# Kernel optimization log

Measured on AMD Instinct MI355X. Metric: run time of the kernel, lower is better.

Reference implementation:

```python
import jax, jax.numpy as jnp
import numpy as np

B, N, DIN, DOUT, DOP = 64, 512, 256, 256, 64
LN_EPS = 1e-5
NEG_SLOPE = 0.2


def setup_inputs() -> dict:
    key = jax.random.key(0)
    ks = jax.random.split(key, 16)
    stdv = 1.0 / np.sqrt(DOUT)

    def lin(k, shape, fan_in):
        # torch nn.Linear default init: U(-1/sqrt(fan_in), 1/sqrt(fan_in))
        bound = 1.0 / np.sqrt(fan_in)
        return jax.random.uniform(k, shape, jnp.float32, -bound, bound)

    return {
        "inputs": jax.random.normal(ks[0], (B, N, DIN), jnp.float32),
        "adj": jax.random.uniform(ks[1], (B, N, N), jnp.float32),
        "op_emb": jax.random.normal(ks[2], (B, N, DOP), jnp.float32),
        # DenseGraphFlow params
        "dgf_W": jax.random.uniform(ks[3], (DIN, DOUT), jnp.float32, -stdv, stdv),
        "dgf_b": jax.random.uniform(ks[4], (DOUT,), jnp.float32, -stdv, stdv),
        "dgf_opW": lin(ks[5], (DOUT, DOP), DOP),
        "dgf_opb": lin(ks[6], (DOUT,), DOP),
        # GraphAttentionLayer params
        "Wk": lin(ks[7], (DOUT, DIN), DIN),
        "Wv": lin(ks[8], (DOUT, DIN), DIN),
        "Wq": lin(ks[9], (DOUT, DIN), DIN),
        "a_w": lin(ks[10], (DOUT,), DOUT),
        "gat_opW": lin(ks[11], (DOUT, DOP), DOP),
        "gat_opb": lin(ks[12], (DOUT,), DOP),
        "ln_g": jnp.ones((DOUT,), jnp.float32),
        "ln_b": jnp.zeros((DOUT,), jnp.float32),
    }


def reference(inputs, adj, op_emb, dgf_W, dgf_b, dgf_opW, dgf_opb,
              Wk, Wv, Wq, a_w, gat_opW, gat_opb, ln_g, ln_b):
    # ----- DenseGraphFlow branch -----
    support = jnp.einsum('bni,io->bno', inputs, dgf_W)            # [B,N,DOUT]
    gate_d = jax.nn.sigmoid(op_emb @ dgf_opW.T + dgf_opb)        # [B,N,DOUT]
    dense = gate_d * jnp.einsum('bij,bjo->bio', adj, support)
    dense = dense + support + dgf_b                               # residual + bias

    # ----- GraphAttentionLayer branch -----
    Whk = inputs @ Wk.T                                           # [B,N,DOUT]
    Whv = inputs @ Wv.T
    Whq = inputs @ Wq.T
    # torch einsum 'balm,beam->belm' (a=1) builds Whq[b,e,:]*Whk[b,l,:];
    # a(.) contracts the feature dim -> equivalent fused score:
    scores = jnp.einsum('bem,blm,m->bel', Whq, Whk, a_w)
    scores = scores / jnp.sqrt(jnp.float32(DOUT))                 # attention_rescale
    alpha = jax.nn.leaky_relu(scores, NEG_SLOPE) * adj            # mask by multiply
    attn = jax.nn.softmax(alpha, axis=-1)                         # softmax over l (neighbors)
    gate_g = jax.nn.sigmoid(op_emb @ gat_opW.T + gat_opb)
    h_prime = gate_g * jnp.einsum('bel,blm->bem', attn, Whv)
    # LayerNorm over last dim
    mu = jnp.mean(h_prime, axis=-1, keepdims=True)
    var = jnp.var(h_prime, axis=-1, keepdims=True)
    gat = (h_prime - mu) * jax.lax.rsqrt(var + LN_EPS) * ln_g + ln_b

    return (dense + gat) * 0.5
```

## Files before the change

### kernel.cpp

```cpp
#include <hip/hip_runtime.h>
#include <cstdint>
#include <cstddef>

typedef unsigned short u16;
typedef unsigned int   u32;
typedef __attribute__((ext_vector_type(8))) short bf16x8;
typedef __attribute__((ext_vector_type(4))) float f32x4;

#define MFMA16(a,b,c) __builtin_amdgcn_mfma_f32_16x16x32_bf16((a),(b),(c),0,0,0)

__device__ __forceinline__ float bf2f(u16 h){
  union { u32 u; float f; } v; v.u = ((u32)h) << 16; return v.f;
}
__device__ __forceinline__ u16 f2bf(float f){
  union { float f; u32 u; } v; v.f = f;
  u32 u = v.u + 0x7FFFu + ((v.u >> 16) & 1u);
  return (u16)(u >> 16);
}
__device__ __forceinline__ float ldf(const void* p, int i, u32 isf32){
  return isf32 ? ((const float*)p)[i] : bf2f(((const u16*)p)[i]);
}

__global__ void kD_detect(const u16* __restrict__ raw, u32* __restrict__ flag)
{
  const int lane = threadIdx.x & 63;
  const float v = bf2f(raw[lane]);
  const unsigned long long big = __ballot(fabsf(v) > 1.0e6f);
  if (lane == 0) flag[0] = (big != 0ull) ? 1u : 0u;
}

__global__ void kC_conv(const void* __restrict__ src, u16* __restrict__ dst,
                        int n, const u32* __restrict__ flag)
{
  const int i8 = (blockIdx.x * 256 + threadIdx.x) << 3;
  if (i8 >= n) return;
  if (flag[0]) {
    const float4 a = ((const float4*)src)[i8 >> 2];
    const float4 b = ((const float4*)src)[(i8 >> 2) + 1];
    u16 o[8] = { f2bf(a.x), f2bf(a.y), f2bf(a.z), f2bf(a.w),
                 f2bf(b.x), f2bf(b.y), f2bf(b.z), f2bf(b.w) };
    *(uint4*)&dst[i8] = *(const uint4*)o;
  } else {
    ((uint4*)dst)[i8 >> 3] = ((const uint4*)src)[i8 >> 3];
  }
}

__global__ void kP_params(const void* dgf_opW, const void* gat_opW,
                          const void* dgf_b,   const void* dgf_opb,
                          const void* gat_opb, const void* ln_g,
                          const void* ln_b,    u16* __restrict__ PB,
                          const u32* __restrict__ flag)
{
  const int i = blockIdx.x * 256 + threadIdx.x;
  if (i >= 34048) return;
  const u32 f = flag[0];
  float v;
  if      (i < 16384) v = ldf(dgf_opW, i, f);
  else if (i < 32768) v = ldf(gat_opW, i - 16384, f);
  else if (i < 33024) v = ldf(dgf_b,   i - 32768, f);
  else if (i < 33280) v = ldf(dgf_opb, i - 33024, f);
  else if (i < 33536) v = ldf(gat_opb, i - 33280, f);
  else if (i < 33792) v = ldf(ln_g,    i - 33536, f);
  else                v = ldf(ln_b,    i - 33792, f);
  PB[i] = f2bf(v);
}

__global__ void k0_wcat(const void* dgfW, const void* Wk, const void* Wv,
                        const void* Wq, const void* aw, u16* __restrict__ Wcat,
                        const u32* __restrict__ flag)
{
  const int o = blockIdx.x;
  const int i = threadIdx.x;
  const u32 f = flag[0];
  float v;
  if (o < 256)       v = ldf(dgfW, i * 256 + o, f);
  else if (o < 512)  v = ldf(Wk, (o - 256) * 256 + i, f);
  else if (o < 768)  v = ldf(Wv, (o - 512) * 256 + i, f);
  else               v = ldf(Wq, (o - 768) * 256 + i, f) * ldf(aw, o - 768, f) * 0.0625f;
  Wcat[o * 256 + i] = f2bf(v);
}

__global__ __launch_bounds__(256, 2)
void k1_proj(const u16* __restrict__ X, const u16* __restrict__ W,
             u16* __restrict__ P, u16* __restrict__ T)
{
  __shared__ __align__(16) u16 ldsA[128 * 64];
  __shared__ __align__(16) u16 ldsB[128 * 64];
  const int bt = blockIdx.x;
  const int ct = blockIdx.y;
  const int r0 = bt << 7;
  const bool swapped = (ct == 4) | (ct == 5) | (ct >= 8);
  const int wbase = (ct < 8) ? (ct << 7) : ((ct - 8) << 7);
  const int tid = threadIdx.x;
  const int wave = tid >> 6;
  const int lane = tid & 63;
  const int wm = wave >> 1, wn = wave & 1;

  f32x4 acc[4][4];
#pragma unroll
  for (int i = 0; i < 4; ++i)
#pragma unroll
    for (int j = 0; j < 4; ++j) acc[i][j] = f32x4{0.f, 0.f, 0.f, 0.f};

  for (int kt = 0; kt < 4; ++kt) {
    __syncthreads();
#pragma unroll
    for (int s = 0; s < 4; ++s) {
      const int slot = ((wave * 4 + s) << 6) + lane;
      const int m = slot >> 3, c = slot & 7;
      const int kb = c ^ (m & 7);
      *(uint4*)&ldsA[slot << 3] =
          *(const uint4*)(X + (r0 + m) * 256 + (kt << 6) + (kb << 3));
      *(uint4*)&ldsB[slot << 3] =
          *(const uint4*)(W + (wbase + m) * 256 + (kt << 6) + (kb << 3));
    }
    __syncthreads();
#pragma unroll
    for (int ks = 0; ks < 2; ++ks) {
      const int kb = (ks << 2) + (lane >> 4);
      bf16x8 fa[4], fb[4];
#pragma unroll
      for (int i = 0; i < 4; ++i) {
        const int m = (wm << 6) + (i << 4) + (lane & 15);
        fa[i] = *(const bf16x8*)&ldsA[((m << 3) + (kb ^ (m & 7))) << 3];
        const int n = (wn << 6) + (i << 4) + (lane & 15);
        fb[i] = *(const bf16x8*)&ldsB[((n << 3) + (kb ^ (n & 7))) << 3];
      }
      if (!swapped) {
#pragma unroll
        for (int i = 0; i < 4; ++i)
#pragma unroll
          for (int j = 0; j < 4; ++j)
            acc[i][j] = MFMA16(fa[i], fb[j], acc[i][j]);
      } else {
#pragma unroll
        for (int i = 0; i < 4; ++i)
#pragma unroll
          for (int j = 0; j < 4; ++j)
            acc[i][j] = MFMA16(fb[i], fa[j], acc[i][j]);
      }
    }
  }

  if (!swapped) {
    const int pcb = (ct < 4) ? (ct << 7) : ((ct - 2) << 7);
#pragma unroll
    for (int i = 0; i < 4; ++i) {
      const int row = r0 + (wm << 6) + (i << 4) + ((lane >> 4) << 2);
#pragma unroll
      for (int j = 0; j < 4; ++j) {
        const int col = pcb + (wn << 6) + (j << 4) + (lane & 15);
#pragma unroll
        for (int r = 0; r < 4; ++r)
          P[(row + r) * 768 + col] = f2bf(acc[i][j][r]);
      }
    }
  } else {
    const int trb = (wbase >= 512) ? (wbase - 256) : wbase;
    const int b = r0 >> 9;
    const int e0 = r0 & 511;
    u16* Tb = T + ((size_t)b << 18);
#pragma unroll
    for (int i = 0; i < 4; ++i) {
      const int trow = trb + (wn << 6) + (i << 4) + ((lane >> 4) << 2);
#pragma unroll
      for (int j = 0; j < 4; ++j) {
        const int e = e0 + (wm << 6) + (j << 4) + (lane & 15);
#pragma unroll
        for (int r = 0; r < 4; ++r)
          Tb[((trow + r) << 9) + e] = f2bf(acc[i][j][r]);
      }
    }
  }
}

__global__ __launch_bounds__(256, 2)
void k2_gates(const u16* __restrict__ OP, const u16* __restrict__ PB,
              u16* __restrict__ G)
{
  __shared__ __align__(16) u16 ldsA[128 * 64];
  __shared__ __align__(16) u16 ldsB[128 * 64];
  const int bt = blockIdx.x, ct = blockIdx.y;
  const int r0 = bt << 7;
  const u16* Wp = (ct < 2) ? (PB + (ct << 7) * 64) : (PB + 16384 + ((ct - 2) << 7) * 64);
  const u16* Bp = (ct < 2) ? (PB + 33024 + (ct << 7)) : (PB + 33280 + ((ct - 2) << 7));
  const int tid = threadIdx.x, wave = tid >> 6, lane = tid & 63;
  const int wm = wave >> 1, wn = wave & 1;

  f32x4 acc[4][4];
#pragma unroll
  for (int i = 0; i < 4; ++i)
#pragma unroll
    for (int j = 0; j < 4; ++j) acc[i][j] = f32x4{0.f, 0.f, 0.f, 0.f};

#pragma unroll
  for (int s = 0; s < 4; ++s) {
    const int slot = ((wave * 4 + s) << 6) + lane;
    const int m = slot >> 3, c = slot & 7;
    const int kb = c ^ (m & 7);
    *(uint4*)&ldsA[slot << 3] = *(const uint4*)(OP + (r0 + m) * 64 + (kb << 3));
    *(uint4*)&ldsB[slot << 3] = *(const uint4*)(Wp + m * 64 + (kb << 3));
  }
  __syncthreads();
#pragma unroll
  for (int ks = 0; ks < 2; ++ks) {
    const int kb = (ks << 2) + (lane >> 4);
    bf16x8 fa[4], fb[4];
#pragma unroll
    for (int i = 0; i < 4; ++i) {
      const int m = (wm << 6) + (i << 4) + (lane & 15);
      fa[i] = *(const bf16x8*)&ldsA[((m << 3) + (kb ^ (m & 7))) << 3];
      const int n = (wn << 6) + (i << 4) + (lane & 15);
      fb[i] = *(const bf16x8*)&ldsB[((n << 3) + (kb ^ (n & 7))) << 3];
    }
#pragma unroll
    for (int i = 0; i < 4; ++i)
#pragma unroll
      for (int j = 0; j < 4; ++j)
        acc[i][j] = MFMA16(fa[i], fb[j], acc[i][j]);
  }
#pragma unroll
  for (int i = 0; i < 4; ++i) {
    const int row = r0 + (wm << 6) + (i << 4) + ((lane >> 4) << 2);
#pragma unroll
    for (int j = 0; j < 4; ++j) {
      const int cw = (wn << 6) + (j << 4) + (lane & 15);
      const float bias = bf2f(Bp[cw]);
      const int col = (ct << 7) + cw;
#pragma unroll
      for (int r = 0; r < 4; ++r) {
        const float x = acc[i][j][r] + bias;
        G[((row + r) << 9) + col] = f2bf(1.0f / (1.0f + __expf(-x)));
      }
    }
  }
}

__global__ __launch_bounds__(256, 2)
void k3_scores(const u16* __restrict__ P, const u16* __restrict__ adj,
               u16* __restrict__ E)
{
  __shared__ __align__(16) u16 ldsA[128 * 64];
  __shared__ __align__(16) u16 ldsB[128 * 64];
  const int lt = blockIdx.x, et = blockIdx.y, b = blockIdx.z;
  const int e0 = et << 7, l0 = lt << 7;
  const int tid = threadIdx.x, wave = tid >> 6, lane = tid & 63;
  const int wm = wave >> 1, wn = wave & 1;
  const int rowQ = (b << 9) + e0;
  const int rowK = (b << 9) + l0;

  f32x4 acc[4][4];
#pragma unroll
  for (int i = 0; i < 4; ++i)
#pragma unroll
    for (int j = 0; j < 4; ++j) acc[i][j] = f32x4{0.f, 0.f, 0.f, 0.f};

  for (int kt = 0; kt < 4; ++kt) {
    __syncthreads();
#pragma unroll
    for (int s = 0; s < 4; ++s) {
      const int slot = ((wave * 4 + s) << 6) + lane;
      const int m = slot >> 3, c = slot & 7;
      const int kb = c ^ (m & 7);
      *(uint4*)&ldsA[slot << 3] =
          *(const uint4*)(P + (rowQ + m) * 768 + 512 + (kt << 6) + (kb << 3));
      *(uint4*)&ldsB[slot << 3] =
          *(const uint4*)(P + (rowK + m) * 768 + 256 + (kt << 6) + (kb << 3));
    }
    __syncthreads();
#pragma unroll
    for (int ks = 0; ks < 2; ++ks) {
      const int kb = (ks << 2) + (lane >> 4);
      bf16x8 fa[4], fb[4];
#pragma unroll
      for (int i = 0; i < 4; ++i) {
        const int m = (wm << 6) + (i << 4) + (lane & 15);
        fa[i] = *(const bf16x8*)&ldsA[((m << 3) + (kb ^ (m & 7))) << 3];
        const int n = (wn << 6) + (i << 4) + (lane & 15);
        fb[i] = *(const bf16x8*)&ldsB[((n << 3) + (kb ^ (n & 7))) << 3];
      }
#pragma unroll
      for (int i = 0; i < 4; ++i)
#pragma unroll
        for (int j = 0; j < 4; ++j)
          acc[i][j] = MFMA16(fa[i], fb[j], acc[i][j]);
    }
  }
#pragma unroll
  for (int i = 0; i < 4; ++i) {
    const int e = e0 + (wm << 6) + (i << 4) + ((lane >> 4) << 2);
#pragma unroll
    for (int j = 0; j < 4; ++j) {
      const int l = l0 + (wn << 6) + (j << 4) + (lane & 15);
#pragma unroll
      for (int r = 0; r < 4; ++r) {
        const int idx = (((b << 9) + e + r) << 9) + l;
        const float a = bf2f(adj[idx]);
        float s = acc[i][j][r];
        s = (s > 0.0f ? s : 0.2f * s) * a;
        E[idx] = f2bf(__expf(s));
      }
    }
  }
}

__global__ void k3b_rowsum(const u16* __restrict__ E, float* __restrict__ S)
{
  const int row = (blockIdx.x << 2) + (threadIdx.x >> 6);
  const int lane = threadIdx.x & 63;
  const uint4 v = *(const uint4*)(const void*)(E + ((size_t)row << 9) + (lane << 3));
  float s = 0.0f;
  const u32 w[4] = {v.x, v.y, v.z, v.w};
#pragma unroll
  for (int q = 0; q < 4; ++q)
    s += bf2f((u16)(w[q] & 0xFFFFu)) + bf2f((u16)(w[q] >> 16));
#pragma unroll
  for (int m = 32; m >= 1; m >>= 1) s += __shfl_xor(s, m, 64);
  if (lane == 0) S[row] = s;
}

__global__ __launch_bounds__(256, 2)
void k4_out(const u16* __restrict__ P, const u16* __restrict__ T,
            const u16* __restrict__ E, const u16* __restrict__ adj,
            const float* __restrict__ S, const u16* __restrict__ G,
            const u16* __restrict__ PB, void* __restrict__ out,
            const u32* __restrict__ flag)
{
  __shared__ __align__(16) u16 ldsA[64 * 64];
  __shared__ __align__(16) u16 ldsB[256 * 64];
  __shared__ float red[64][4];
  const int et = blockIdx.x, b = blockIdx.y;
  const int e0 = et << 6;
  const int tid = threadIdx.x, wave = tid >> 6, lane = tid & 63;
  const int wm = wave >> 1, wn = wave & 1;
  const size_t abase = ((size_t)((b << 9) + e0)) << 9;
  const u16* Ea  = E + abase;
  const u16* Aa  = adj + abase;
  const u16* Tb  = T + ((size_t)b << 18);
  const u16* WhvT = Tb + (256 << 9);
  const u16* SupT = Tb;
  const u16* dgf_b = PB + 32768;
  const u16* ln_g  = PB + 33536;
  const u16* ln_b  = PB + 33792;
  const u32 isf32 = flag[0];

  f32x4 acc[2][2][8];
#pragma unroll
  for (int p = 0; p < 2; ++p)
#pragma unroll
    for (int i = 0; i < 2; ++i)
#pragma unroll
      for (int j = 0; j < 8; ++j) acc[p][i][j] = f32x4{0.f, 0.f, 0.f, 0.f};

#pragma unroll
  for (int ph = 0; ph < 2; ++ph) {
    const u16* Ag = ph ? Aa : Ea;
    const u16* Bg = ph ? SupT : WhvT;
    for (int lt = 0; lt < 8; ++lt) {
      __syncthreads();
#pragma unroll
      for (int s2 = 0; s2 < 2; ++s2) {
        const int slot = ((wave * 2 + s2) << 6) + lane;
        const int m = slot >> 3, c = slot & 7;
        const int kb = c ^ (m & 7);
        *(uint4*)&ldsA[slot << 3] =
            *(const uint4*)(Ag + (m << 9) + (lt << 6) + (kb << 3));
      }
#pragma unroll
      for (int s2 = 0; s2 < 8; ++s2) {
        const int slot = ((wave * 8 + s2) << 6) + lane;
        const int m = slot >> 3, c = slot & 7;
        const int kb = c ^ (m & 7);
        *(uint4*)&ldsB[slot << 3] =
            *(const uint4*)(Bg + (m << 9) + (lt << 6) + (kb << 3));
      }
      __syncthreads();
#pragma unroll
      for (int ks = 0; ks < 2; ++ks) {
        const int kb = (ks << 2) + (lane >> 4);
        bf16x8 fa[2];
#pragma unroll
        for (int i = 0; i < 2; ++i) {
          const int m = (wm << 5) + (i << 4) + (lane & 15);
          fa[i] = *(const bf16x8*)&ldsA[((m << 3) + (kb ^ (m & 7))) << 3];
        }
#pragma unroll
        for (int j = 0; j < 8; ++j) {
          const int n = (wn << 7) + (j << 4) + (lane & 15);
          const bf16x8 fb = *(const bf16x8*)&ldsB[((n << 3) + (kb ^ (n & 7))) << 3];
          acc[ph][0][j] = MFMA16(fa[0], fb, acc[ph][0][j]);
          acc[ph][1][j] = MFMA16(fa[1], fb, acc[ph][1][j]);
        }
      }
    }
  }

  const int cb = wn << 7;
  float lng[8], lnb[8], dgb[8];
#pragma unroll
  for (int j = 0; j < 8; ++j) {
    const int col = cb + (j << 4) + (lane & 15);
    lng[j] = bf2f(ln_g[col]);
    lnb[j] = bf2f(ln_b[col]);
    dgb[j] = bf2f(dgf_b[col]);
  }
#pragma unroll
  for (int i = 0; i < 2; ++i) {
#pragma unroll
    for (int r = 0; r < 4; ++r) {
      const int rl = (wm << 5) + (i << 4) + ((lane >> 4) << 2) + r;
      const int grow = (b << 9) + e0 + rl;
      const float invS = 1.0f / S[grow];
      float ps = 0.0f, pq = 0.0f;
#pragma unroll
      for (int j = 0; j < 8; ++j) {
        const int col = cb + (j << 4) + (lane & 15);
        const float gg = bf2f(G[((size_t)grow << 9) + 256 + col]);
        const float hp = gg * acc[0][i][j][r] * invS;
        acc[0][i][j][r] = hp;
        ps += hp; pq += hp * hp;
      }
#pragma unroll
      for (int m = 1; m < 16; m <<= 1) {
        ps += __shfl_xor(ps, m, 64);
        pq += __shfl_xor(pq, m, 64);
      }
      if ((lane & 15) == 0) { red[rl][wn << 1] = ps; red[rl][(wn << 1) + 1] = pq; }
    }
  }
  __syncthreads();
#pragma unroll
  for (int i = 0; i < 2; ++i) {
#pragma unroll
    for (int r = 0; r < 4; ++r) {
      const int rl = (wm << 5) + (i << 4) + ((lane >> 4) << 2) + r;
      const int grow = (b << 9) + e0 + rl;
      const float mean = (red[rl][0] + red[rl][2]) * (1.0f / 256.0f);
      const float ex2  = (red[rl][1] + red[rl][3]) * (1.0f / 256.0f);
      const float rstd = rsqrtf(ex2 - mean * mean + 1e-5f);
#pragma unroll
      for (int j = 0; j < 8; ++j) {
        const int col = cb + (j << 4) + (lane & 15);
        const float gat = (acc[0][i][j][r] - mean) * rstd * lng[j] + lnb[j];
        const float gd = bf2f(G[((size_t)grow << 9) + col]);
        const float sup = bf2f(P[grow * 768 + col]);
        const float dense = gd * acc[1][i][j][r] + sup + dgb[j];
        const float o = 0.5f * (dense + gat);
        if (isf32) ((float*)out)[grow * 256 + col] = o;
        else       ((u16*)out)[grow * 256 + col] = f2bf(o);
      }
    }
  }
}

extern "C" void kernel_launch(void* const* d_in, const int* in_sizes, int n_in,
                              void* d_out, int out_size, void* d_ws, size_t ws_size,
                              hipStream_t stream)
{
  (void)in_sizes; (void)n_in; (void)out_size; (void)ws_size;
  const void* inputs  = d_in[0];
  const void* adj     = d_in[1];
  const void* op_emb  = d_in[2];
  const void* dgf_W   = d_in[3];
  const void* dgf_b   = d_in[4];
  const void* dgf_opW = d_in[5];
  const void* dgf_opb = d_in[6];
  const void* Wk      = d_in[7];
  const void* Wv      = d_in[8];
  const void* Wq      = d_in[9];
  const void* a_w     = d_in[10];
  const void* gat_opW = d_in[11];
  const void* gat_opb = d_in[12];
  const void* ln_g    = d_in[13];
  const void* ln_b    = d_in[14];
  char* ws = (char*)d_ws;

  u16*  P    = (u16*)(ws);
  u16*  T    = (u16*)(ws + 50331648ull);
  u16*  E    = (u16*)(ws + 83886080ull);
  u16*  G    = (u16*)(ws + 117440512ull);
  u16*  Cadj = (u16*)(ws + 150994944ull);
  u16*  Cin  = (u16*)(ws + 184549376ull);
  u16*  Cop  = (u16*)(ws + 201326592ull);
  u16*  Wcat = (u16*)(ws + 205520896ull);
  u16*  PB   = (u16*)(ws + 206045184ull);
  float* Srw = (float*)(ws + 206114816ull);
  u32*  flag = (u32*)(ws + 206245888ull);

  kD_detect <<<dim3(1),       dim3(64),  0, stream>>>((const u16*)inputs, flag);
  kC_conv   <<<dim3(4096),    dim3(256), 0, stream>>>(inputs, Cin,  8388608, flag);
  kC_conv   <<<dim3(1024),    dim3(256), 0, stream>>>(op_emb, Cop,  2097152, flag);
  kC_conv   <<<dim3(8192),    dim3(256), 0, stream>>>(adj,    Cadj, 16777216, flag);
  kP_params <<<dim3(134),     dim3(256), 0, stream>>>(dgf_opW, gat_opW, dgf_b,
                                                      dgf_opb, gat_opb, ln_g, ln_b,
                                                      PB, flag);
  k0_wcat   <<<dim3(1024),    dim3(256), 0, stream>>>(dgf_W, Wk, Wv, Wq, a_w,
                                                      Wcat, flag);
  k1_proj   <<<dim3(256, 10), dim3(256), 0, stream>>>(Cin, Wcat, P, T);
  k2_gates  <<<dim3(256, 4),  dim3(256), 0, stream>>>(Cop, PB, G);
  k3_scores <<<dim3(4, 4, 64),dim3(256), 0, stream>>>(P, Cadj, E);
  k3b_rowsum<<<dim3(8192),    dim3(256), 0, stream>>>(E, Srw);
  k4_out    <<<dim3(8, 64),   dim3(256), 0, stream>>>(P, T, E, Cadj, Srw, G,
                                                      PB, d_out, flag);
}
```

Before: 332.1 us.

## Fuse softmax row-sum into output GEMM and load MFMA fragments directly

Removes the separate row-sum kernel and computes the softmax denominator inside k4_out with an extra MFMA against a vector of ones. The output kernel now uses 32-row tiles (twice as many blocks), drops LDS staging and reads MFMA fragments straight from global memory, and fuses the two GEMM phases into one K loop. This saves a launch and a full re-read of E and raises occupancy. The cost is uncoalesced global fragment loads with no LDS reuse, so the B operands are fetched more often from cache.

```diff
diff --git a/kernel.cpp b/kernel.cpp
--- a/kernel.cpp
+++ b/kernel.cpp
@@ -304,120 +304,102 @@
   }
 }
 
-__global__ void k3b_rowsum(const u16* __restrict__ E, float* __restrict__ S)
-{
-  const int row = (blockIdx.x << 2) + (threadIdx.x >> 6);
-  const int lane = threadIdx.x & 63;
-  const uint4 v = *(const uint4*)(const void*)(E + ((size_t)row << 9) + (lane << 3));
-  float s = 0.0f;
-  const u32 w[4] = {v.x, v.y, v.z, v.w};
-#pragma unroll
-  for (int q = 0; q < 4; ++q)
-    s += bf2f((u16)(w[q] & 0xFFFFu)) + bf2f((u16)(w[q] >> 16));
-#pragma unroll
-  for (int m = 32; m >= 1; m >>= 1) s += __shfl_xor(s, m, 64);
-  if (lane == 0) S[row] = s;
-}
-
-__global__ __launch_bounds__(256, 2)
+__global__ __launch_bounds__(256, 3)
 void k4_out(const u16* __restrict__ P, const u16* __restrict__ T,
             const u16* __restrict__ E, const u16* __restrict__ adj,
-            const float* __restrict__ S, const u16* __restrict__ G,
-            const u16* __restrict__ PB, void* __restrict__ out,
-            const u32* __restrict__ flag)
-{
-  __shared__ __align__(16) u16 ldsA[64 * 64];
-  __shared__ __align__(16) u16 ldsB[256 * 64];
-  __shared__ float red[64][4];
+            const u16* __restrict__ G, const u16* __restrict__ PB,
+            void* __restrict__ out, const u32* __restrict__ flag)
+{
+  __shared__ float red[32][8];
   const int et = blockIdx.x, b = blockIdx.y;
-  const int e0 = et << 6;
-  const int tid = threadIdx.x, wave = tid >> 6, lane = tid & 63;
-  const int wm = wave >> 1, wn = wave & 1;
+  const int e0 = et << 5;
+  const int tid = threadIdx.x;
+  const int wn = tid >> 6;
+  const int lane = tid & 63;
+  const int lr = lane & 15;
+  const int kc = (lane >> 4) << 3;
   const size_t abase = ((size_t)((b << 9) + e0)) << 9;
-  const u16* Ea  = E + abase;
-  const u16* Aa  = adj + abase;
-  const u16* Tb  = T + ((size_t)b << 18);
-  const u16* WhvT = Tb + (256 << 9);
-  const u16* SupT = Tb;
+
+  const u16* pE[2]; const u16* pA[2]; const u16* pBv[4]; const u16* pBs[4];
+#pragma unroll
+  for (int i = 0; i < 2; ++i) {
+    const size_t ro = abase + ((size_t)((i << 4) + lr) << 9) + kc;
+    pE[i] = E + ro;
+    pA[i] = adj + ro;
+  }
+  const u16* Tb = T + ((size_t)b << 18);
+#pragma unroll
+  for (int j = 0; j < 4; ++j) {
+    const int n = (wn << 6) + (j << 4) + lr;
+    pBv[j] = Tb + ((size_t)(256 + n) << 9) + kc;
+    pBs[j] = Tb + ((size_t)n << 9) + kc;
+  }
+
+  f32x4 acc0[2][4], acc1[2][4], accS[2];
+#pragma unroll
+  for (int i = 0; i < 2; ++i) {
+    accS[i] = f32x4{0.f, 0.f, 0.f, 0.f};
+#pragma unroll
+    for (int j = 0; j < 4; ++j) {
+      acc0[i][j] = f32x4{0.f, 0.f, 0.f, 0.f};
+      acc1[i][j] = f32x4{0.f, 0.f, 0.f, 0.f};
+    }
+  }
+  const short onebf = (short)0x3F80;
+  const bf16x8 ones = {onebf, onebf, onebf, onebf, onebf, onebf, onebf, onebf};
+
+  for (int ks = 0; ks < 16; ++ks) {
+    const int off = ks << 5;
+    bf16x8 fae[2], faa[2], fbv[4], fbs[4];
+#pragma unroll
+    for (int i = 0; i < 2; ++i) {
+      fae[i] = *(const bf16x8*)(pE[i] + off);
+      faa[i] = *(const bf16x8*)(pA[i] + off);
+    }
+#pragma unroll
+    for (int j = 0; j < 4; ++j) {
+      fbv[j] = *(const bf16x8*)(pBv[j] + off);
+      fbs[j] = *(const bf16x8*)(pBs[j] + off);
+    }
+#pragma unroll
+    for (int i = 0; i < 2; ++i) {
+#pragma unroll
+      for (int j = 0; j < 4; ++j) {
+        acc0[i][j] = MFMA16(fae[i], fbv[j], acc0[i][j]);
+        acc1[i][j] = MFMA16(faa[i], fbs[j], acc1[i][j]);
+      }
+      accS[i] = MFMA16(fae[i], ones, accS[i]);
+    }
+  }
+
   const u16* dgf_b = PB + 32768;
   const u16* ln_g  = PB + 33536;
   const u16* ln_b  = PB + 33792;
   const u32 isf32 = flag[0];
 
-  f32x4 acc[2][2][8];
-#pragma unroll
-  for (int p = 0; p < 2; ++p)
-#pragma unroll
-    for (int i = 0; i < 2; ++i)
-#pragma unroll
-      for (int j = 0; j < 8; ++j) acc[p][i][j] = f32x4{0.f, 0.f, 0.f, 0.f};
-
-#pragma unroll
-  for (int ph = 0; ph < 2; ++ph) {
-    const u16* Ag = ph ? Aa : Ea;
-    const u16* Bg = ph ? SupT : WhvT;
-    for (int lt = 0; lt < 8; ++lt) {
-      __syncthreads();
-#pragma unroll
-      for (int s2 = 0; s2 < 2; ++s2) {
-        const int slot = ((wave * 2 + s2) << 6) + lane;
-        const int m = slot >> 3, c = slot & 7;
-        const int kb = c ^ (m & 7);
-        *(uint4*)&ldsA[slot << 3] =
-            *(const uint4*)(Ag + (m << 9) + (lt << 6) + (kb << 3));
-      }
-#pragma unroll
-      for (int s2 = 0; s2 < 8; ++s2) {
-        const int slot = ((wave * 8 + s2) << 6) + lane;
-        const int m = slot >> 3, c = slot & 7;
-        const int kb = c ^ (m & 7);
-        *(uint4*)&ldsB[slot << 3] =
-            *(const uint4*)(Bg + (m << 9) + (lt << 6) + (kb << 3));
-      }
-      __syncthreads();
-#pragma unroll
-      for (int ks = 0; ks < 2; ++ks) {
-        const int kb = (ks << 2) + (lane >> 4);
-        bf16x8 fa[2];
-#pragma unroll
-        for (int i = 0; i < 2; ++i) {
-          const int m = (wm << 5) + (i << 4) + (lane & 15);
-          fa[i] = *(const bf16x8*)&ldsA[((m << 3) + (kb ^ (m & 7))) << 3];
-        }
-#pragma unroll
-        for (int j = 0; j < 8; ++j) {
-          const int n = (wn << 7) + (j << 4) + (lane & 15);
-          const bf16x8 fb = *(const bf16x8*)&ldsB[((n << 3) + (kb ^ (n & 7))) << 3];
-          acc[ph][0][j] = MFMA16(fa[0], fb, acc[ph][0][j]);
-          acc[ph][1][j] = MFMA16(fa[1], fb, acc[ph][1][j]);
-        }
-      }
-    }
-  }
-
-  const int cb = wn << 7;
-  float lng[8], lnb[8], dgb[8];
-#pragma unroll
-  for (int j = 0; j < 8; ++j) {
-    const int col = cb + (j << 4) + (lane & 15);
+  float lng[4], lnb[4], dgb[4];
+#pragma unroll
+  for (int j = 0; j < 4; ++j) {
+    const int col = (wn << 6) + (j << 4) + lr;
     lng[j] = bf2f(ln_g[col]);
     lnb[j] = bf2f(ln_b[col]);
     dgb[j] = bf2f(dgf_b[col]);
   }
+
 #pragma unroll
   for (int i = 0; i < 2; ++i) {
 #pragma unroll
     for (int r = 0; r < 4; ++r) {
-      const int rl = (wm << 5) + (i << 4) + ((lane >> 4) << 2) + r;
+      const int rl = (i << 4) + ((lane >> 4) << 2) + r;
       const int grow = (b << 9) + e0 + rl;
-      const float invS = 1.0f / S[grow];
+      const float invS = 1.0f / accS[i][r];
       float ps = 0.0f, pq = 0.0f;
 #pragma unroll
-      for (int j = 0; j < 8; ++j) {
-        const int col = cb + (j << 4) + (lane & 15);
+      for (int j = 0; j < 4; ++j) {
+        const int col = (wn << 6) + (j << 4) + lr;
         const float gg = bf2f(G[((size_t)grow << 9) + 256 + col]);
-        const float hp = gg * acc[0][i][j][r] * invS;
-        acc[0][i][j][r] = hp;
+        const float hp = gg * acc0[i][j][r] * invS;
+        acc0[i][j][r] = hp;
         ps += hp; pq += hp * hp;
       }
 #pragma unroll
@@ -425,7 +407,7 @@
         ps += __shfl_xor(ps, m, 64);
         pq += __shfl_xor(pq, m, 64);
       }
-      if ((lane & 15) == 0) { red[rl][wn << 1] = ps; red[rl][(wn << 1) + 1] = pq; }
+      if (lr == 0) { red[rl][wn << 1] = ps; red[rl][(wn << 1) + 1] = pq; }
     }
   }
   __syncthreads();
@@ -433,18 +415,18 @@
   for (int i = 0; i < 2; ++i) {
 #pragma unroll
     for (int r = 0; r < 4; ++r) {
-      const int rl = (wm << 5) + (i << 4) + ((lane >> 4) << 2) + r;
+      const int rl = (i << 4) + ((lane >> 4) << 2) + r;
       const int grow = (b << 9) + e0 + rl;
-      const float mean = (red[rl][0] + red[rl][2]) * (1.0f / 256.0f);
-      const float ex2  = (red[rl][1] + red[rl][3]) * (1.0f / 256.0f);
+      const float mean = (red[rl][0] + red[rl][2] + red[rl][4] + red[rl][6]) * (1.0f / 256.0f);
+      const float ex2  = (red[rl][1] + red[rl][3] + red[rl][5] + red[rl][7]) * (1.0f / 256.0f);
       const float rstd = rsqrtf(ex2 - mean * mean + 1e-5f);
 #pragma unroll
-      for (int j = 0; j < 8; ++j) {
-        const int col = cb + (j << 4) + (lane & 15);
-        const float gat = (acc[0][i][j][r] - mean) * rstd * lng[j] + lnb[j];
+      for (int j = 0; j < 4; ++j) {
+        const int col = (wn << 6) + (j << 4) + lr;
+        const float gat = (acc0[i][j][r] - mean) * rstd * lng[j] + lnb[j];
         const float gd = bf2f(G[((size_t)grow << 9) + col]);
         const float sup = bf2f(P[grow * 768 + col]);
-        const float dense = gd * acc[1][i][j][r] + sup + dgb[j];
+        const float dense = gd * acc1[i][j][r] + sup + dgb[j];
         const float o = 0.5f * (dense + gat);
         if (isf32) ((float*)out)[grow * 256 + col] = o;
         else       ((u16*)out)[grow * 256 + col] = f2bf(o);
@@ -484,7 +466,6 @@
   u16*  Cop  = (u16*)(ws + 201326592ull);
   u16*  Wcat = (u16*)(ws + 205520896ull);
   u16*  PB   = (u16*)(ws + 206045184ull);
-  float* Srw = (float*)(ws + 206114816ull);
   u32*  flag = (u32*)(ws + 206245888ull);
 
   kD_detect <<<dim3(1),       dim3(64),  0, stream>>>((const u16*)inputs, flag);
@@ -499,7 +480,6 @@
   k1_proj   <<<dim3(256, 10), dim3(256), 0, stream>>>(Cin, Wcat, P, T);
   k2_gates  <<<dim3(256, 4),  dim3(256), 0, stream>>>(Cop, PB, G);
   k3_scores <<<dim3(4, 4, 64),dim3(256), 0, stream>>>(P, Cadj, E);
-  k3b_rowsum<<<dim3(8192),    dim3(256), 0, stream>>>(E, Srw);
-  k4_out    <<<dim3(8, 64),   dim3(256), 0, stream>>>(P, T, E, Cadj, Srw, G,
+  k4_out    <<<dim3(16, 64),  dim3(256), 0, stream>>>(P, T, E, Cadj, G,
                                                       PB, d_out, flag);
 }
```

After: 385.9 us. 1.16x slower.

## Load GEMM tiles directly into LDS and fold softmax row sums into MFMA

Applied to the files above, without the earlier changes.

Global-to-shared tile loads in the projection, score and output kernels now use direct global_load_lds, avoiding the register round trip, and the per-thread addresses are precomputed outside the k-loop. The separate row-sum kernel is removed. Softmax denominators are instead accumulated in the output kernel with an extra MFMA against a ones vector during the attention phase. This saves one launch and a full pass over E, at the cost of extra MFMAs and reliance on direct-to-LDS load semantics and ordering.

```diff
diff --git a/kernel.cpp b/kernel.cpp
--- a/kernel.cpp
+++ b/kernel.cpp
@@ -19,6 +19,11 @@
 }
 __device__ __forceinline__ float ldf(const void* p, int i, u32 isf32){
   return isf32 ? ((const float*)p)[i] : bf2f(((const u16*)p)[i]);
+}
+__device__ __forceinline__ void gld16(const u16* g, u16* l){
+  __builtin_amdgcn_global_load_lds(
+      (const __attribute__((address_space(1))) void*)g,
+      (__attribute__((address_space(3))) void*)l, 16, 0, 0);
 }
 
 __global__ void kD_detect(const u16* __restrict__ raw, u32* __restrict__ flag)
@@ -96,6 +101,17 @@
   const int lane = tid & 63;
   const int wm = wave >> 1, wn = wave & 1;
 
+  int gA[4], gB[4], dS[4];
+#pragma unroll
+  for (int s = 0; s < 4; ++s) {
+    const int slot = ((wave * 4 + s) << 6) + lane;
+    const int m = slot >> 3, c = slot & 7;
+    const int kb = c ^ (m & 7);
+    gA[s] = (r0 + m) * 256 + (kb << 3);
+    gB[s] = (wbase + m) * 256 + (kb << 3);
+    dS[s] = slot << 3;
+  }
+
   f32x4 acc[4][4];
 #pragma unroll
   for (int i = 0; i < 4; ++i)
@@ -106,13 +122,8 @@
     __syncthreads();
 #pragma unroll
     for (int s = 0; s < 4; ++s) {
-      const int slot = ((wave * 4 + s) << 6) + lane;
-      const int m = slot >> 3, c = slot & 7;
-      const int kb = c ^ (m & 7);
-      *(uint4*)&ldsA[slot << 3] =
-          *(const uint4*)(X + (r0 + m) * 256 + (kt << 6) + (kb << 3));
-      *(uint4*)&ldsB[slot << 3] =
-          *(const uint4*)(W + (wbase + m) * 256 + (kt << 6) + (kb << 3));
+      gld16(X + gA[s] + (kt << 6), &ldsA[dS[s]]);
+      gld16(W + gB[s] + (kt << 6), &ldsB[dS[s]]);
     }
     __syncthreads();
 #pragma unroll
@@ -249,6 +260,17 @@
   const int rowQ = (b << 9) + e0;
   const int rowK = (b << 9) + l0;
 
+  int gA[4], gB[4], dS[4];
+#pragma unroll
+  for (int s = 0; s < 4; ++s) {
+    const int slot = ((wave * 4 + s) << 6) + lane;
+    const int m = slot >> 3, c = slot & 7;
+    const int kb = c ^ (m & 7);
+    gA[s] = (rowQ + m) * 768 + 512 + (kb << 3);
+    gB[s] = (rowK + m) * 768 + 256 + (kb << 3);
+    dS[s] = slot << 3;
+  }
+
   f32x4 acc[4][4];
 #pragma unroll
   for (int i = 0; i < 4; ++i)
@@ -259,13 +281,8 @@
     __syncthreads();
 #pragma unroll
     for (int s = 0; s < 4; ++s) {
-      const int slot = ((wave * 4 + s) << 6) + lane;
-      const int m = slot >> 3, c = slot & 7;
-      const int kb = c ^ (m & 7);
-      *(uint4*)&ldsA[slot << 3] =
-          *(const uint4*)(P + (rowQ + m) * 768 + 512 + (kt << 6) + (kb << 3));
-      *(uint4*)&ldsB[slot << 3] =
-          *(const uint4*)(P + (rowK + m) * 768 + 256 + (kt << 6) + (kb << 3));
+      gld16(P + gA[s] + (kt << 6), &ldsA[dS[s]]);
+      gld16(P + gB[s] + (kt << 6), &ldsB[dS[s]]);
     }
     __syncthreads();
 #pragma unroll
@@ -304,27 +321,11 @@
   }
 }
 
-__global__ void k3b_rowsum(const u16* __restrict__ E, float* __restrict__ S)
-{
-  const int row = (blockIdx.x << 2) + (threadIdx.x >> 6);
-  const int lane = threadIdx.x & 63;
-  const uint4 v = *(const uint4*)(const void*)(E + ((size_t)row << 9) + (lane << 3));
-  float s = 0.0f;
-  const u32 w[4] = {v.x, v.y, v.z, v.w};
-#pragma unroll
-  for (int q = 0; q < 4; ++q)
-    s += bf2f((u16)(w[q] & 0xFFFFu)) + bf2f((u16)(w[q] >> 16));
-#pragma unroll
-  for (int m = 32; m >= 1; m >>= 1) s += __shfl_xor(s, m, 64);
-  if (lane == 0) S[row] = s;
-}
-
 __global__ __launch_bounds__(256, 2)
 void k4_out(const u16* __restrict__ P, const u16* __restrict__ T,
             const u16* __restrict__ E, const u16* __restrict__ adj,
-            const float* __restrict__ S, const u16* __restrict__ G,
-            const u16* __restrict__ PB, void* __restrict__ out,
-            const u32* __restrict__ flag)
+            const u16* __restrict__ G, const u16* __restrict__ PB,
+            void* __restrict__ out, const u32* __restrict__ flag)
 {
   __shared__ __align__(16) u16 ldsA[64 * 64];
   __shared__ __align__(16) u16 ldsB[256 * 64];
@@ -344,13 +345,33 @@
   const u16* ln_b  = PB + 33792;
   const u32 isf32 = flag[0];
 
-  f32x4 acc[2][2][8];
-#pragma unroll
-  for (int p = 0; p < 2; ++p)
-#pragma unroll
-    for (int i = 0; i < 2; ++i)
+  int gA[2], dA[2], gB[8], dB[8];
+#pragma unroll
+  for (int s2 = 0; s2 < 2; ++s2) {
+    const int slot = ((wave * 2 + s2) << 6) + lane;
+    const int m = slot >> 3, c = slot & 7;
+    gA[s2] = (m << 9) + ((c ^ (m & 7)) << 3);
+    dA[s2] = slot << 3;
+  }
+#pragma unroll
+  for (int s2 = 0; s2 < 8; ++s2) {
+    const int slot = ((wave * 8 + s2) << 6) + lane;
+    const int m = slot >> 3, c = slot & 7;
+    gB[s2] = (m << 9) + ((c ^ (m & 7)) << 3);
+    dB[s2] = slot << 3;
+  }
+
+  f32x4 acc[2][2][8], accS[2];
+#pragma unroll
+  for (int i = 0; i < 2; ++i) {
+    accS[i] = f32x4{0.f, 0.f, 0.f, 0.f};
+#pragma unroll
+    for (int p = 0; p < 2; ++p)
 #pragma unroll
       for (int j = 0; j < 8; ++j) acc[p][i][j] = f32x4{0.f, 0.f, 0.f, 0.f};
+  }
+  const short onebf = (short)0x3F80;
+  const bf16x8 ones = {onebf, onebf, onebf, onebf, onebf, onebf, onebf, onebf};
 
 #pragma unroll
   for (int ph = 0; ph < 2; ++ph) {
@@ -359,21 +380,11 @@
     for (int lt = 0; lt < 8; ++lt) {
       __syncthreads();
 #pragma unroll
-      for (int s2 = 0; s2 < 2; ++s2) {
-        const int slot = ((wave * 2 + s2) << 6) + lane;
-        const int m = slot >> 3, c = slot & 7;
-        const int kb = c ^ (m & 7);
-        *(uint4*)&ldsA[slot << 3] =
-            *(const uint4*)(Ag + (m << 9) + (lt << 6) + (kb << 3));
-      }
-#pragma unroll
-      for (int s2 = 0; s2 < 8; ++s2) {
-        const int slot = ((wave * 8 + s2) << 6) + lane;
-        const int m = slot >> 3, c = slot & 7;
-        const int kb = c ^ (m & 7);
-        *(uint4*)&ldsB[slot << 3] =
-            *(const uint4*)(Bg + (m << 9) + (lt << 6) + (kb << 3));
-      }
+      for (int s2 = 0; s2 < 2; ++s2)
+        gld16(Ag + gA[s2] + (lt << 6), &ldsA[dA[s2]]);
+#pragma unroll
+      for (int s2 = 0; s2 < 8; ++s2)
+        gld16(Bg + gB[s2] + (lt << 6), &ldsB[dB[s2]]);
       __syncthreads();
 #pragma unroll
       for (int ks = 0; ks < 2; ++ks) {
@@ -391,6 +402,10 @@
           acc[ph][0][j] = MFMA16(fa[0], fb, acc[ph][0][j]);
           acc[ph][1][j] = MFMA16(fa[1], fb, acc[ph][1][j]);
         }
+        if (ph == 0) {
+          accS[0] = MFMA16(fa[0], ones, accS[0]);
+          accS[1] = MFMA16(fa[1], ones, accS[1]);
+        }
       }
     }
   }
@@ -410,7 +425,7 @@
     for (int r = 0; r < 4; ++r) {
       const int rl = (wm << 5) + (i << 4) + ((lane >> 4) << 2) + r;
       const int grow = (b << 9) + e0 + rl;
-      const float invS = 1.0f / S[grow];
+      const float invS = 1.0f / accS[i][r];
       float ps = 0.0f, pq = 0.0f;
 #pragma unroll
       for (int j = 0; j < 8; ++j) {
@@ -484,7 +499,6 @@
   u16*  Cop  = (u16*)(ws + 201326592ull);
   u16*  Wcat = (u16*)(ws + 205520896ull);
   u16*  PB   = (u16*)(ws + 206045184ull);
-  float* Srw = (float*)(ws + 206114816ull);
   u32*  flag = (u32*)(ws + 206245888ull);
 
   kD_detect <<<dim3(1),       dim3(64),  0, stream>>>((const u16*)inputs, flag);
@@ -499,7 +513,6 @@
   k1_proj   <<<dim3(256, 10), dim3(256), 0, stream>>>(Cin, Wcat, P, T);
   k2_gates  <<<dim3(256, 4),  dim3(256), 0, stream>>>(Cop, PB, G);
   k3_scores <<<dim3(4, 4, 64),dim3(256), 0, stream>>>(P, Cadj, E);
-  k3b_rowsum<<<dim3(8192),    dim3(256), 0, stream>>>(E, Srw);
-  k4_out    <<<dim3(8, 64),   dim3(256), 0, stream>>>(P, T, E, Cadj, Srw, G,
+  k4_out    <<<dim3(8, 64),   dim3(256), 0, stream>>>(P, T, E, Cadj, G,
                                                       PB, d_out, flag);
 }
```

Measured after the change: 323.5 us. -2.6%, faster.
